# Kernel optimization log

Hardware: AMD Instinct MI355X
Metric: run time of the kernel (lower is better)

## Reference

```python
import math
import jax, jax.numpy as jnp
import numpy as np

B, T, D = 128, 243, 1024   # batch, motion frames, latent_dim
N, L = 77, 512             # text tokens, text_latent_dim
H = 16                     # num_head -> head_dim 64
EPS = 1e-5


def _ln(x, g, b):
    m = x.mean(-1, keepdims=True)
    v = jnp.var(x, axis=-1, keepdims=True)
    return (x - m) * jax.lax.rsqrt(v + EPS) * g + b


def setup_inputs() -> dict:
    key = jax.random.key(0)
    ks = jax.random.split(key, 16)
    s = 0.02
    return {
        "x": jax.random.normal(ks[0], (B, T, D), jnp.float32),
        "xf": jax.random.normal(ks[1], (B, N, L), jnp.float32),
        "emb": jax.random.normal(ks[2], (B, T, D), jnp.float32),
        "ln_g": jnp.ones((D,), jnp.float32), "ln_b": jnp.zeros((D,), jnp.float32),
        "tln_g": jnp.ones((L,), jnp.float32), "tln_b": jnp.zeros((L,), jnp.float32),
        "Wq": jax.random.normal(ks[3], (D, D), jnp.float32) * s,
        "bq": jnp.zeros((D,), jnp.float32),
        "Wk": jax.random.normal(ks[4], (L, D), jnp.float32) * s,
        "bk": jnp.zeros((D,), jnp.float32),
        "Wv": jax.random.normal(ks[5], (L, D), jnp.float32) * s,
        "bv": jnp.zeros((D,), jnp.float32),
        "We": jax.random.normal(ks[6], (D, 2 * D), jnp.float32) * s,  # emb_layers Linear(time_embed_dim=D, 2D)
        "be": jnp.zeros((2 * D,), jnp.float32),
        "ln2_g": jnp.ones((D,), jnp.float32), "ln2_b": jnp.zeros((D,), jnp.float32),
        "Wo": jax.random.normal(ks[7], (D, D), jnp.float32) * s,     # zero_module in torch; random here for non-trivial baseline
        "bo": jnp.zeros((D,), jnp.float32),
    }


def reference(x, xf, emb, ln_g, ln_b, tln_g, tln_b, Wq, bq, Wk, bk, Wv, bv,
              We, be, ln2_g, ln2_b, Wo, bo):
    B_, T_, D_ = x.shape
    dh = D_ // H
    # cross-attention: queries from motion tokens, keys/values from text
    q = (_ln(x, ln_g, ln_b) @ Wq + bq).reshape(B_, T_, H, dh)
    xfn = _ln(xf, tln_g, tln_b)
    k = (xfn @ Wk + bk).reshape(B_, -1, H, dh)
    v = (xfn @ Wv + bv).reshape(B_, -1, H, dh)
    att = jnp.einsum('bthd,bnhd->btnh', q, k) / math.sqrt(dh)  # (B,T,N,H)
    w = jax.nn.softmax(att, axis=2)                            # softmax over text tokens; dropout is eval-mode identity
    y = jnp.einsum('btnh,bnhd->bthd', w, v).reshape(B_, T_, D_)
    # StylizationBlock (AdaLN): emb viewed (B,T,D), only first timestep used
    emb_out = (jax.nn.silu(emb) @ We + be)[:, 0:1, :]          # (B,1,2D)
    scale, shift = jnp.split(emb_out, 2, axis=2)
    h = _ln(y, ln2_g, ln2_b) * (1.0 + scale) + shift
    h = jax.nn.silu(h) @ Wo + bo
    return x + h
```

## Files before the change

kernel.cpp:

```cpp
#include <hip/hip_runtime.h>
#include <cstdint>

typedef __attribute__((ext_vector_type(8))) __bf16 bf16x8;
typedef __attribute__((ext_vector_type(4))) float f32x4;
typedef __attribute__((ext_vector_type(8))) unsigned short ushort8v;

__device__ __forceinline__ float b2f(unsigned short u) {
    union { uint32_t i; float f; } w; w.i = ((uint32_t)u) << 16; return w.f;
}
__device__ __forceinline__ unsigned short f2b(float f) {
    union { uint32_t i; float f; } w; w.f = f;
    uint32_t r = (w.i + 0x7FFFu + ((w.i >> 16) & 1u)) >> 16;
    return (unsigned short)r;
}

__device__ __forceinline__ void gl16(const unsigned short* g, unsigned short* l) {
    __builtin_amdgcn_global_load_lds(
        (const __attribute__((address_space(1))) void*)g,
        (__attribute__((address_space(3))) void*)l,
        16, 0, 0);
}

__device__ __forceinline__ int swz8(int wg, int nwg) {
    const int q = nwg >> 3, r = nwg & 7;
    const int xcd = wg & 7, idx = wg >> 3;
    return (xcd < r) ? (xcd * (q + 1) + idx)
                     : (r * (q + 1) + (xcd - r) * q + idx);
}

template <int DIM>
__device__ __forceinline__ void ln_body(int bid, const float* __restrict__ in,
                                        const float* __restrict__ g,
                                        const float* __restrict__ b,
                                        unsigned short* __restrict__ out) {
    const int row = bid * 4 + (threadIdx.x >> 6);
    const int ln = threadIdx.x & 63;
    constexpr int PL = DIM / 64;
    float v[PL];
    const size_t base = (size_t)row * DIM + (size_t)ln * PL;
    const float4* p4 = (const float4*)(in + base);
#pragma unroll
    for (int c = 0; c < PL / 4; ++c) {
        const float4 t = p4[c];
        v[c * 4 + 0] = t.x; v[c * 4 + 1] = t.y; v[c * 4 + 2] = t.z; v[c * 4 + 3] = t.w;
    }
    float s = 0.f, s2 = 0.f;
#pragma unroll
    for (int c = 0; c < PL; ++c) { s += v[c]; s2 += v[c] * v[c]; }
    for (int o = 1; o < 64; o <<= 1) { s += __shfl_xor(s, o); s2 += __shfl_xor(s2, o); }
    const float mean = s / DIM;
    const float rstd = rsqrtf(s2 / DIM - mean * mean + 1e-5f);
    const float* gp = g + ln * PL;
    const float* bp = b + ln * PL;
#pragma unroll
    for (int c0 = 0; c0 < PL; c0 += 8) {
        ushort8v yv;
#pragma unroll
        for (int j = 0; j < 8; ++j) {
            const int c = c0 + j;
            yv[j] = f2b((v[c] - mean) * rstd * gp[c] + bp[c]);
        }
        *(ushort8v*)(out + base + c0) = yv;
    }
}

__global__ __launch_bounds__(256) void k_pre(
    const float* __restrict__ x, const float* __restrict__ ln_g, const float* __restrict__ ln_b,
    unsigned short* __restrict__ xn,
    const float* __restrict__ xf, const float* __restrict__ tln_g, const float* __restrict__ tln_b,
    unsigned short* __restrict__ xfn,
    const float* __restrict__ emb, unsigned short* __restrict__ se,
    const float* __restrict__ Wq, const float* __restrict__ Wk,
    const float* __restrict__ Wv, const float* __restrict__ We,
    const float* __restrict__ Wo,
    unsigned short* __restrict__ wqt, unsigned short* __restrict__ wkvt,
    unsigned short* __restrict__ wet, unsigned short* __restrict__ wot) {
    __shared__ float s[32][33];
    int bid = blockIdx.x;
    if (bid < 7776) { ln_body<1024>(bid, x, ln_g, ln_b, xn); return; }
    bid -= 7776;
    if (bid < 2464) { ln_body<512>(bid, xf, tln_g, tln_b, xfn); return; }
    bid -= 2464;
    if (bid < 512) {
        const int i = bid * 256 + threadIdx.x;
        const int b = i >> 10, k = i & 1023;
        const float f = emb[(size_t)b * (243 * 1024) + k];
        se[i] = f2b(f / (1.f + __expf(-f)));
        return;
    }
    bid -= 512;
    const float* in; unsigned short* out; int R, C;
    if (bid < 1024)      { in = Wq; out = wqt;              R = 1024; C = 1024; }
    else if (bid < 1536) { bid -= 1024; in = Wk; out = wkvt;             R = 512;  C = 1024; }
    else if (bid < 2048) { bid -= 1536; in = Wv; out = wkvt + 1024 * 512; R = 512;  C = 1024; }
    else if (bid < 4096) { bid -= 2048; in = We; out = wet;              R = 1024; C = 2048; }
    else                 { bid -= 4096; in = Wo; out = wot;              R = 1024; C = 1024; }
    const int ctiles = C >> 5;
    const int c0 = (bid % ctiles) * 32, r0 = (bid / ctiles) * 32;
    const int tx = threadIdx.x & 31, ty = threadIdx.x >> 5;
#pragma unroll
    for (int i = 0; i < 4; ++i)
        s[ty + i * 8][tx] = in[(size_t)(r0 + ty + i * 8) * C + c0 + tx];
    __syncthreads();
#pragma unroll
    for (int i = 0; i < 4; ++i)
        out[(size_t)(c0 + ty + i * 8) * R + r0 + tx] = f2b(s[tx][ty + i * 8]);
}

__device__ __forceinline__ void mm_body(
    int u, int NN,
    const unsigned short* __restrict__ A, const unsigned short* __restrict__ Bt,
    const float* __restrict__ bias0, const float* __restrict__ bias1,
    unsigned short* __restrict__ C0, unsigned short* __restrict__ C1,
    float* __restrict__ Cf, const float* __restrict__ X,
    int N, int K, int epi,
    unsigned short* sA, unsigned short* sB) {
    const int tid = threadIdx.x, wv = tid >> 6, ln = tid & 63;
    const int wm = wv >> 2, wn = wv & 3;
    const int ln15 = ln & 15, lg = ln >> 4;
    const int m0 = (u / NN) * 128, n0 = (u % NN) * 256;

    const f32x4 fz = {0.f, 0.f, 0.f, 0.f};
    f32x4 acc[4][4];
#pragma unroll
    for (int i = 0; i < 4; ++i)
#pragma unroll
        for (int j = 0; j < 4; ++j) acc[i][j] = fz;

    const int lrow = ln >> 3;
    const int sslot = (ln & 7) ^ lrow;
    const unsigned short* ga = A + (size_t)(m0 + wv * 16 + lrow) * K + sslot * 8;
    const unsigned short* gb = Bt + (size_t)(n0 + wv * 32 + lrow) * K + sslot * 8;
    unsigned short* const lA = sA + (wv * 16) * 64;
    unsigned short* const lB = sB + (wv * 32) * 64;

    for (int k0 = 0; k0 < K; k0 += 64) {
#pragma unroll
        for (int i = 0; i < 2; ++i)
            gl16(ga + k0 + (size_t)i * 8 * K, lA + i * 8 * 64);
#pragma unroll
        for (int i = 0; i < 4; ++i)
            gl16(gb + k0 + (size_t)i * 8 * K, lB + i * 8 * 64);
        __syncthreads();
        bf16x8 af[4][2], bf[4][2];
#pragma unroll
        for (int i = 0; i < 4; ++i) {
            const int ra2 = wm * 64 + i * 16 + ln15;
            const int rb2 = wn * 64 + i * 16 + ln15;
#pragma unroll
            for (int ks = 0; ks < 2; ++ks) {
                const int slot = ks * 4 + lg;
                af[i][ks] = *(const bf16x8*)(sA + ra2 * 64 + ((slot ^ (ra2 & 7)) * 8));
                bf[i][ks] = *(const bf16x8*)(sB + rb2 * 64 + ((slot ^ (rb2 & 7)) * 8));
            }
        }
#pragma unroll
        for (int mi = 0; mi < 4; ++mi)
#pragma unroll
            for (int ni = 0; ni < 4; ++ni) {
                acc[mi][ni] = __builtin_amdgcn_mfma_f32_16x16x32_bf16(af[mi][0], bf[ni][0], acc[mi][ni], 0, 0, 0);
                acc[mi][ni] = __builtin_amdgcn_mfma_f32_16x16x32_bf16(af[mi][1], bf[ni][1], acc[mi][ni], 0, 0, 0);
            }
        __syncthreads();
    }

    const int colB = n0 + wn * 64;
    const int rowB = m0 + wm * 64;
#pragma unroll
    for (int mi = 0; mi < 4; ++mi) {
#pragma unroll
        for (int ni = 0; ni < 4; ++ni) {
            const int col = colB + ni * 16 + ln15;
            const int row = rowB + mi * 16 + lg * 4;
            float bvv;
            if (epi == 2) bvv = (col < 1024) ? bias0[col] : bias1[col - 1024];
            else bvv = bias0[col];
#pragma unroll
            for (int r2 = 0; r2 < 4; ++r2) {
                const float v = acc[mi][ni][r2] + bvv;
                if (epi == 0) {
                    C0[(size_t)(row + r2) * N + col] = f2b(v);
                } else if (epi == 1) {
                    Cf[(size_t)(row + r2) * N + col] = v + X[(size_t)(row + r2) * N + col];
                } else if (epi == 2) {
                    if (col < 1024) C0[(size_t)(row + r2) * 1024 + col] = f2b(v);
                    else C1[(size_t)(row + r2) * 1024 + (col - 1024)] = f2b(v);
                } else {
                    Cf[(size_t)(row + r2) * N + col] = v;
                }
            }
        }
    }
}

__global__ __launch_bounds__(512, 2) void k_mm3(
    const unsigned short* __restrict__ xn, const unsigned short* __restrict__ wqt,
    const float* __restrict__ bq, unsigned short* __restrict__ qb,
    const unsigned short* __restrict__ xfn, const unsigned short* __restrict__ wkvt,
    const float* __restrict__ bk, const float* __restrict__ bv,
    unsigned short* __restrict__ kb, unsigned short* __restrict__ vb,
    const unsigned short* __restrict__ se, const unsigned short* __restrict__ wet,
    const float* __restrict__ be, float* __restrict__ eo) {
    __shared__ __align__(16) unsigned short sA[128 * 64];
    __shared__ __align__(16) unsigned short sB[256 * 64];
    const int wg = blockIdx.x;
    if (wg < 972) {
        mm_body(swz8(wg, 972), 4, xn, wqt, bq, nullptr, qb, nullptr, nullptr, nullptr,
                1024, 1024, 0, sA, sB);
    } else if (wg < 1588) {
        mm_body(swz8(wg - 972, 616), 8, xfn, wkvt, bk, bv, kb, vb, nullptr, nullptr,
                2048, 512, 2, sA, sB);
    } else {
        mm_body(wg - 1588, 8, se, wet, be, nullptr, nullptr, nullptr, eo, nullptr,
                2048, 1024, 3, sA, sB);
    }
}

__global__ __launch_bounds__(512, 2) void k_mm1(
    const unsigned short* __restrict__ actb, const unsigned short* __restrict__ wot,
    const float* __restrict__ bo, const float* __restrict__ x,
    float* __restrict__ outp) {
    __shared__ __align__(16) unsigned short sA[128 * 64];
    __shared__ __align__(16) unsigned short sB[256 * 64];
    mm_body(swz8(blockIdx.x, 972), 4, actb, wot, bo, nullptr, nullptr, nullptr,
            outp, x, 1024, 1024, 1, sA, sB);
}

__global__ __launch_bounds__(256, 2) void k_attn_m(const unsigned short* __restrict__ Q,
                                                   const unsigned short* __restrict__ Kb,
                                                   const unsigned short* __restrict__ Vb,
                                                   unsigned short* __restrict__ Y) {
    __shared__ __align__(16) unsigned short sK[80 * 64];
    __shared__ __align__(16) unsigned short sV[64 * 96];
    __shared__ __align__(16) unsigned short sU[4 * 16 * 104];
    unsigned short* const sVr = sU;
    const int bh = blockIdx.x;
    const int b = bh >> 4, h = bh & 15;
    const int tid = threadIdx.x, wv = tid >> 6, ln = tid & 63;
    const int ln15 = ln & 15, lg = ln >> 4;
    unsigned short* const sP = sU + wv * (16 * 104);

    for (int c = tid; c < 640; c += 256) {
        const int n = c >> 3, ci = c & 7;
        uint4 kv = make_uint4(0u, 0u, 0u, 0u), vv = make_uint4(0u, 0u, 0u, 0u);
        if (n < 77) {
            const size_t o = (size_t)(b * 77 + n) * 1024 + h * 64 + ci * 8;
            kv = *(const uint4*)(Kb + o);
            vv = *(const uint4*)(Vb + o);
        }
        *(uint4*)((char*)sK + n * 128 + ((ci * 16) ^ ((n & 7) << 4))) = kv;
        *(uint4*)(sVr + n * 72 + ci * 8) = vv;
    }
    bf16x8 qf[4][2];
    const size_t qbase = (size_t)b * (243 * 1024) + h * 64;
#pragma unroll
    for (int mi = 0; mi < 4; ++mi) {
        int t = wv * 64 + mi * 16 + ln15;
        if (t > 242) t = 242;
#pragma unroll
        for (int ks = 0; ks < 2; ++ks)
            qf[mi][ks] = *(const bf16x8*)(Q + qbase + (size_t)t * 1024 + ks * 32 + lg * 8);
    }
    __syncthreads();

    for (int i = tid; i < 64 * 96; i += 256) {
        const int d = i / 96, n = i - d * 96;
        sV[i] = (n < 80) ? sVr[n * 72 + d] : (unsigned short)0;
    }
    __syncthreads();

    for (int i = ln; i < 16 * 24; i += 64) {
        const int rr = i / 24, cc = i - rr * 24;
        sP[rr * 104 + 80 + cc] = 0;
    }

    const f32x4 fz = {0.f, 0.f, 0.f, 0.f};
#pragma unroll
    for (int mi = 0; mi < 4; ++mi) {
        f32x4 sc[5];
#pragma unroll
        for (int ci = 0; ci < 5; ++ci) sc[ci] = fz;
        __builtin_amdgcn_s_setprio(1);
#pragma unroll
        for (int ci = 0; ci < 5; ++ci) {
            const int n = ci * 16 + ln15;
#pragma unroll
            for (int ks = 0; ks < 2; ++ks) {
                const int kk = ks * 32 + lg * 8;
                bf16x8 kf = *(const bf16x8*)((const char*)sK + n * 128 + ((kk * 2) ^ ((n & 7) << 4)));
                sc[ci] = __builtin_amdgcn_mfma_f32_16x16x32_bf16(qf[mi][ks], kf, sc[ci], 0, 0, 0);
            }
        }
        __builtin_amdgcn_s_setprio(0);
#pragma unroll
        for (int r = 0; r < 4; ++r) {
            float e[5];
            float mx = -1e30f;
#pragma unroll
            for (int ci = 0; ci < 5; ++ci) {
                const int n = ci * 16 + ln15;
                const float vv = (n < 77) ? sc[ci][r] * 0.125f : -1e30f;
                e[ci] = vv;
                mx = fmaxf(mx, vv);
            }
            mx = fmaxf(mx, __shfl_xor(mx, 1));
            mx = fmaxf(mx, __shfl_xor(mx, 2));
            mx = fmaxf(mx, __shfl_xor(mx, 4));
            mx = fmaxf(mx, __shfl_xor(mx, 8));
            float ssum = 0.f;
#pragma unroll
            for (int ci = 0; ci < 5; ++ci) {
                const int n = ci * 16 + ln15;
                const float ev = (n < 77) ? __expf(e[ci] - mx) : 0.f;
                e[ci] = ev;
                ssum += ev;
            }
            ssum += __shfl_xor(ssum, 1);
            ssum += __shfl_xor(ssum, 2);
            ssum += __shfl_xor(ssum, 4);
            ssum += __shfl_xor(ssum, 8);
            const float inv = 1.f / ssum;
            const int prow = lg * 4 + r;
#pragma unroll
            for (int ci = 0; ci < 5; ++ci)
                sP[prow * 104 + ci * 16 + ln15] = f2b(e[ci] * inv);
        }
        f32x4 ya[4];
#pragma unroll
        for (int di = 0; di < 4; ++di) ya[di] = fz;
        __builtin_amdgcn_s_setprio(1);
#pragma unroll
        for (int ks = 0; ks < 3; ++ks) {
            bf16x8 pa = *(const bf16x8*)(sP + ln15 * 104 + ks * 32 + lg * 8);
#pragma unroll
            for (int di = 0; di < 4; ++di) {
                bf16x8 vf = *(const bf16x8*)(sV + (di * 16 + ln15) * 96 + ks * 32 + lg * 8);
                ya[di] = __builtin_amdgcn_mfma_f32_16x16x32_bf16(pa, vf, ya[di], 0, 0, 0);
            }
        }
        __builtin_amdgcn_s_setprio(0);
        unsigned short* sy = sP;
#pragma unroll
        for (int di = 0; di < 4; ++di)
#pragma unroll
            for (int r = 0; r < 4; ++r)
                sy[(lg * 4 + r) * 72 + di * 16 + ln15] = f2b(ya[di][r]);
        const int tb = wv * 64 + mi * 16;
#pragma unroll
        for (int j = 0; j < 2; ++j) {
            const int k = ln * 2 + j;
            const int row = k >> 3, off = (k & 7) * 8;
            const int t = tb + row;
            if (t < 243)
                *(uint4*)(Y + qbase + (size_t)t * 1024 + off) = *(const uint4*)(sy + row * 72 + off);
        }
    }
}

__global__ __launch_bounds__(256) void k_act(const unsigned short* __restrict__ y,
                                             const float* __restrict__ eo,
                                             const float* __restrict__ g,
                                             const float* __restrict__ b,
                                             unsigned short* __restrict__ out) {
    const int row = blockIdx.x * 4 + (threadIdx.x >> 6);
    const int ln = threadIdx.x & 63;
    const int bb = row / 243;
    float v[16];
    const size_t base = (size_t)row * 1024 + ln * 16;
#pragma unroll
    for (int c0 = 0; c0 < 16; c0 += 8) {
        const ushort8v t = *(const ushort8v*)(y + base + c0);
#pragma unroll
        for (int j = 0; j < 8; ++j) v[c0 + j] = b2f(t[j]);
    }
    float s = 0.f, s2 = 0.f;
#pragma unroll
    for (int c = 0; c < 16; ++c) { s += v[c]; s2 += v[c] * v[c]; }
    for (int o = 1; o < 64; o <<= 1) { s += __shfl_xor(s, o); s2 += __shfl_xor(s2, o); }
    const float mean = s / 1024.f;
    const float rstd = rsqrtf(s2 / 1024.f - mean * mean + 1e-5f);
    const float* gp = g + ln * 16;
    const float* bp = b + ln * 16;
    const float* sc = eo + (size_t)bb * 2048 + ln * 16;
    const float* sh = sc + 1024;
#pragma unroll
    for (int c0 = 0; c0 < 16; c0 += 8) {
        ushort8v yv;
#pragma unroll
        for (int j = 0; j < 8; ++j) {
            const int c = c0 + j;
            const float nl = (v[c] - mean) * rstd * gp[c] + bp[c];
            const float hh = nl * (1.f + sc[c]) + sh[c];
            yv[j] = f2b(hh / (1.f + __expf(-hh)));
        }
        *(ushort8v*)(out + base + c0) = yv;
    }
}

extern "C" void kernel_launch(void* const* d_in, const int* in_sizes, int n_in,
                              void* d_out, int out_size, void* d_ws, size_t ws_size,
                              hipStream_t stream) {
    (void)in_sizes; (void)n_in; (void)out_size; (void)ws_size;

    const float* x     = (const float*)d_in[0];
    const float* xf    = (const float*)d_in[1];
    const float* emb   = (const float*)d_in[2];
    const float* ln_g  = (const float*)d_in[3];
    const float* ln_b  = (const float*)d_in[4];
    const float* tln_g = (const float*)d_in[5];
    const float* tln_b = (const float*)d_in[6];
    const float* Wq    = (const float*)d_in[7];
    const float* bq    = (const float*)d_in[8];
    const float* Wk    = (const float*)d_in[9];
    const float* bk    = (const float*)d_in[10];
    const float* Wv    = (const float*)d_in[11];
    const float* bv    = (const float*)d_in[12];
    const float* We    = (const float*)d_in[13];
    const float* be    = (const float*)d_in[14];
    const float* ln2_g = (const float*)d_in[15];
    const float* ln2_b = (const float*)d_in[16];
    const float* Wo    = (const float*)d_in[17];
    const float* bo    = (const float*)d_in[18];
    float* outp = (float*)d_out;

    char* ws = (char*)d_ws;
    constexpr size_t o_wq   = 0;
    constexpr size_t o_wkv  = o_wq + 2097152;
    constexpr size_t o_we   = o_wkv + 2097152;
    constexpr size_t o_wo   = o_we + 4194304;
    constexpr size_t o_se   = o_wo + 2097152;
    constexpr size_t o_eo   = o_se + 262144;
    constexpr size_t o_xn   = o_eo + 1048576;
    constexpr size_t o_qb   = o_xn + 63700992;
    constexpr size_t o_xfn  = o_qb + 63700992;
    constexpr size_t o_kb   = o_xfn + 10092544;
    constexpr size_t o_vb   = o_kb + 20185088;

    unsigned short* wqt  = (unsigned short*)(ws + o_wq);
    unsigned short* wkvt = (unsigned short*)(ws + o_wkv);
    unsigned short* wet  = (unsigned short*)(ws + o_we);
    unsigned short* wot  = (unsigned short*)(ws + o_wo);
    unsigned short* se   = (unsigned short*)(ws + o_se);
    float*          eo   = (float*)(ws + o_eo);
    unsigned short* xn   = (unsigned short*)(ws + o_xn);
    unsigned short* yb   = xn;
    unsigned short* qb   = (unsigned short*)(ws + o_qb);
    unsigned short* actb = qb;
    unsigned short* xfn  = (unsigned short*)(ws + o_xfn);
    unsigned short* kb   = (unsigned short*)(ws + o_kb);
    unsigned short* vb   = (unsigned short*)(ws + o_vb);

    k_pre<<<15872, 256, 0, stream>>>(x, ln_g, ln_b, xn,
                                     xf, tln_g, tln_b, xfn,
                                     emb, se,
                                     Wq, Wk, Wv, We, Wo,
                                     wqt, wkvt, wet, wot);

    k_mm3<<<1596, 512, 0, stream>>>(xn, wqt, bq, qb,
                                    xfn, wkvt, bk, bv, kb, vb,
                                    se, wet, be, eo);

    k_attn_m<<<2048, 256, 0, stream>>>(qb, kb, vb, yb);

    k_act<<<7776, 256, 0, stream>>>(yb, eo, ln2_g, ln2_b, actb);

    k_mm1<<<972, 512, 0, stream>>>(actb, wot, bo, x, outp);
}
```

Measured before the change: 340.4 us.

## Double-buffer LDS tiles in GEMM mainloop with async prefetch two stages ahead

```diff
diff --git a/kernel.cpp b/kernel.cpp
--- a/kernel.cpp
+++ b/kernel.cpp
@@ -131,17 +131,29 @@
     const int sslot = (ln & 7) ^ lrow;
     const unsigned short* ga = A + (size_t)(m0 + wv * 16 + lrow) * K + sslot * 8;
     const unsigned short* gb = Bt + (size_t)(n0 + wv * 32 + lrow) * K + sslot * 8;
-    unsigned short* const lA = sA + (wv * 16) * 64;
-    unsigned short* const lB = sB + (wv * 32) * 64;
-
-    for (int k0 = 0; k0 < K; k0 += 64) {
+
+    const int NT = K >> 6;
+    auto STAGE = [&](int t, int buf) {
+        const int k0 = t << 6;
+        unsigned short* const lA = sA + buf * (128 * 64) + (wv * 16) * 64;
+        unsigned short* const lB = sB + buf * (256 * 64) + (wv * 32) * 64;
 #pragma unroll
         for (int i = 0; i < 2; ++i)
             gl16(ga + k0 + (size_t)i * 8 * K, lA + i * 8 * 64);
 #pragma unroll
         for (int i = 0; i < 4; ++i)
             gl16(gb + k0 + (size_t)i * 8 * K, lB + i * 8 * 64);
-        __syncthreads();
+    };
+
+    STAGE(0, 0);
+    STAGE(1, 1);
+    asm volatile("s_waitcnt vmcnt(6)" ::: "memory");
+    __builtin_amdgcn_s_barrier();
+
+    for (int t = 0; t < NT; ++t) {
+        const int cur = t & 1;
+        const unsigned short* bA = sA + cur * (128 * 64);
+        const unsigned short* bB = sB + cur * (256 * 64);
         bf16x8 af[4][2], bf[4][2];
 #pragma unroll
         for (int i = 0; i < 4; ++i) {
@@ -150,10 +162,11 @@
 #pragma unroll
             for (int ks = 0; ks < 2; ++ks) {
                 const int slot = ks * 4 + lg;
-                af[i][ks] = *(const bf16x8*)(sA + ra2 * 64 + ((slot ^ (ra2 & 7)) * 8));
-                bf[i][ks] = *(const bf16x8*)(sB + rb2 * 64 + ((slot ^ (rb2 & 7)) * 8));
-            }
-        }
+                af[i][ks] = *(const bf16x8*)(bA + ra2 * 64 + ((slot ^ (ra2 & 7)) * 8));
+                bf[i][ks] = *(const bf16x8*)(bB + rb2 * 64 + ((slot ^ (rb2 & 7)) * 8));
+            }
+        }
+        __builtin_amdgcn_s_setprio(1);
 #pragma unroll
         for (int mi = 0; mi < 4; ++mi)
 #pragma unroll
@@ -161,7 +174,17 @@
                 acc[mi][ni] = __builtin_amdgcn_mfma_f32_16x16x32_bf16(af[mi][0], bf[ni][0], acc[mi][ni], 0, 0, 0);
                 acc[mi][ni] = __builtin_amdgcn_mfma_f32_16x16x32_bf16(af[mi][1], bf[ni][1], acc[mi][ni], 0, 0, 0);
             }
-        __syncthreads();
+        __builtin_amdgcn_s_setprio(0);
+        asm volatile("s_waitcnt lgkmcnt(0)" ::: "memory");
+        __builtin_amdgcn_s_barrier();
+        if (t + 2 < NT) {
+            STAGE(t + 2, cur);
+            asm volatile("s_waitcnt vmcnt(6)" ::: "memory");
+            __builtin_amdgcn_s_barrier();
+        } else if (t + 1 < NT) {
+            asm volatile("s_waitcnt vmcnt(0)" ::: "memory");
+            __builtin_amdgcn_s_barrier();
+        }
     }
 
     const int colB = n0 + wn * 64;
@@ -201,8 +224,8 @@
     unsigned short* __restrict__ kb, unsigned short* __restrict__ vb,
     const unsigned short* __restrict__ se, const unsigned short* __restrict__ wet,
     const float* __restrict__ be, float* __restrict__ eo) {
-    __shared__ __align__(16) unsigned short sA[128 * 64];
-    __shared__ __align__(16) unsigned short sB[256 * 64];
+    __shared__ __align__(16) unsigned short sA[2 * 128 * 64];
+    __shared__ __align__(16) unsigned short sB[2 * 256 * 64];
     const int wg = blockIdx.x;
     if (wg < 972) {
         mm_body(swz8(wg, 972), 4, xn, wqt, bq, nullptr, qb, nullptr, nullptr, nullptr,
@@ -220,8 +243,8 @@
     const unsigned short* __restrict__ actb, const unsigned short* __restrict__ wot,
     const float* __restrict__ bo, const float* __restrict__ x,
     float* __restrict__ outp) {
-    __shared__ __align__(16) unsigned short sA[128 * 64];
-    __shared__ __align__(16) unsigned short sB[256 * 64];
+    __shared__ __align__(16) unsigned short sA[2 * 128 * 64];
+    __shared__ __align__(16) unsigned short sB[2 * 256 * 64];
     mm_body(swz8(blockIdx.x, 972), 4, actb, wot, bo, nullptr, nullptr, nullptr,
             outp, x, 1024, 1024, 1, sA, sB);
 }
```

Measured after the change: 395.2 us. 1.16x slower.
